# Kernel optimization log

Measured on AMD Instinct MI355X. Metric: run time of the kernel, lower is better.

## Reference

```python
import jax, jax.numpy as jnp
import numpy as np

LAPLACIAN = jnp.array([[-1., -1., -1.], [-1., 8., -1.], [-1., -1., -1.]], dtype=jnp.float32).reshape(1, 1, 3, 3)
AVG5 = jnp.ones((1, 1, 5, 5), dtype=jnp.float32) / 25.0


def _conv_same(x, kernel):
    # x: [B,1,H,W], kernel: [O=1,I=1,kh,kw], SAME padding (odd kernels)
    return jax.lax.conv_general_dilated(
        x, kernel, window_strides=(1, 1), padding='SAME',
        dimension_numbers=('NCHW', 'OIHW', 'NCHW'))


def setup_inputs() -> dict:
    key = jax.random.key(0)
    k0, k1, k2, k3 = jax.random.split(key, 4)
    B, H, W = 16, 1024, 1024
    mask = jax.random.uniform(k0, (B, 1, H, W), dtype=jnp.float32)
    # per-sample params scaled into documented ranges
    blur_strength = 1.0 + 4.0 * jax.random.uniform(k1, (B, 1), dtype=jnp.float32)      # 1.0-5.0
    edge_sensitivity = 0.5 + 1.5 * jax.random.uniform(k2, (B, 1), dtype=jnp.float32)   # 0.5-2.0
    final_threshold = 0.3 + 0.4 * jax.random.uniform(k3, (B, 1), dtype=jnp.float32)    # 0.3-0.7
    return {"mask": mask, "blur_strength": blur_strength,
            "edge_sensitivity": edge_sensitivity, "final_threshold": final_threshold}


def reference(mask, blur_strength, edge_sensitivity, final_threshold):
    B = mask.shape[0]
    edges = jnp.abs(_conv_same(mask, LAPLACIAN))                      # [B,1,H,W]
    edge_threshold = 0.5 * edge_sensitivity.reshape(B, 1, 1, 1)
    edge_mask = (edges > edge_threshold).astype(mask.dtype)
    smoothed_base = _conv_same(mask, AVG5)                            # 5x5 box blur
    blur_factor = blur_strength.reshape(B, 1, 1, 1) / 3.0
    smoothed = mask * (1.0 - blur_factor) + smoothed_base * blur_factor
    result = mask * (1.0 - edge_mask) + smoothed * edge_mask
    final_mask = (result > final_threshold.reshape(B, 1, 1, 1)).astype(mask.dtype)
    return final_mask
```

## Files before the change

kernel.cpp:

```cpp
#include <hip/hip_runtime.h>

#define NB 16
#define HH 1024
#define WW 1024
#define TW 128
#define TH 32
#define LC 136
#define LR 36
#define N4 (LR * (LC / 4))
#define NSTG 5

#define EPS1 2e-4f
#define EPS2 1e-4f

typedef float f32x4 __attribute__((ext_vector_type(4)));

__device__ __noinline__ float aes_exact(const float (*raw)[LC], int lr, int lc,
                                        float bsf, float esf, float fthr)
{
    const double bfd   = (double)bsf / 3.0;
    const double ethrd = 0.5 * (double)esf;
    const double fthrd = (double)fthr;
    const double w25d  = (double)(1.0f / 25.0f);

    double s25 = 0.0, s9 = 0.0;
    for (int dy = 0; dy < 5; ++dy)
        for (int dx = 0; dx < 5; ++dx) {
            double v = (double)raw[lr + dy][lc + dx];
            s25 += v;
            if (dy >= 1 && dy <= 3 && dx >= 1 && dx <= 3) s9 += v;
        }
    double c      = (double)raw[lr + 2][lc + 2];
    double edges  = fabs(9.0 * c - s9);
    double sbase  = s25 * w25d;
    double smooth = c * (1.0 - bfd) + sbase * bfd;
    double result = (edges > ethrd) ? smooth : c;
    return (result > fthrd) ? 1.0f : 0.0f;
}

__global__ __launch_bounds__(256)
void aes_kernel(const float* __restrict__ mask,
                const float* __restrict__ blur_strength,
                const float* __restrict__ edge_sensitivity,
                const float* __restrict__ final_threshold,
                float* __restrict__ out)
{
    __shared__ float raw[2][LR][LC];

    const int b      = blockIdx.z;
    const int tile_y = blockIdx.y * TH;
    const int tx0    = blockIdx.x * (2 * TW);
    const float* m = mask + (size_t)b * (HH * WW);

    const float bsf    = blur_strength[b];
    const float esf    = edge_sensitivity[b];
    const float fthr   = final_threshold[b];
    const float ethr   = 0.5f * esf;
    const float bff    = bsf / 3.0f;
    const float onembf = 1.0f - bff;
    const float w25f   = 1.0f / 25.0f;

    const int tx  = threadIdx.x & 31;
    const int ty  = threadIdx.x >> 5;
    const int lr0 = ty * 4;
    const int lc0 = 4 * tx + 2;

    f32x4 stg[NSTG];

#define STAGE_LOAD(TILE_X)                                                  \
    {                                                                       \
        _Pragma("unroll")                                                   \
        for (int k = 0; k < NSTG; ++k) {                                    \
            int i = (int)threadIdx.x + k * 256;                             \
            f32x4 v = {0.f, 0.f, 0.f, 0.f};                                 \
            if (i < N4) {                                                   \
                int row = i / (LC / 4);                                     \
                int c4  = i - row * (LC / 4);                               \
                int gy  = tile_y - 2 + row;                                 \
                int gx  = (TILE_X) - 4 + 4 * c4;           \
                if ((unsigned)gy < (unsigned)HH && (unsigned)gx < (unsigned)WW) \
                    v = *(const f32x4*)(m + (size_t)gy * WW + gx);          \
            }                                                               \
            stg[k] = v;                                                     \
        }                                                                   \
    }

#define STAGE_WRITE(BUF)                                                    \
    {                                                                       \
        _Pragma("unroll")                                                   \
        for (int k = 0; k < NSTG; ++k) {                                    \
            int i = (int)threadIdx.x + k * 256;                             \
            if (i < N4) {                                                   \
                int row = i / (LC / 4);                                     \
                int c4  = i - row * (LC / 4);                               \
                *(f32x4*)&raw[(BUF)][row][4 * c4] = stg[k];                 \
            }                                                               \
        }                                                                   \
    }

#define LOADROW(RB, ROWIDX, K)                                              \
    {                                                                       \
        const float* rp = &RB[(ROWIDX)][0];                                 \
        float2 u0 = *(const float2*)(rp + lc0);            \
        float4 u1 = *(const float4*)(rp + lc0 + 2);        \
        float2 u2 = *(const float2*)(rp + lc0 + 6);        \
        float a0 = u0.x, a1 = u0.y, a2 = u1.x, a3 = u1.y;                   \
        float a4 = u1.z, a5 = u1.w, a6 = u2.x, a7 = u2.y;                   \
        float s5 = ((a0 + a1) + (a2 + a3)) + a4;                            \
        h5[(K)][0] = s5; s5 = s5 - a0 + a5;                                 \
        h5[(K)][1] = s5; s5 = s5 - a1 + a6;                                 \
        h5[(K)][2] = s5; s5 = s5 - a2 + a7;                                 \
        h5[(K)][3] = s5;                                                    \
        float s3 = (a1 + a2) + a3;                                          \
        h3[(K)][0] = s3; s3 = s3 - a1 + a4;                                 \
        h3[(K)][1] = s3; s3 = s3 - a2 + a5;                                 \
        h3[(K)][2] = s3; s3 = s3 - a3 + a6;                                 \
        h3[(K)][3] = s3;                                                    \
        cc[(K)][0] = a2; cc[(K)][1] = a3; cc[(K)][2] = a4; cc[(K)][3] = a5; \
    }

#define COMPUTE(BUF, TILE_X)                                                \
    {                                                                       \
        const float (*rb)[LC] = raw[(BUF)];                                 \
        float h5[5][4], h3[5][4], cc[5][4];                                 \
        _Pragma("unroll")                                                   \
        for (int k = 0; k < 4; ++k)                                         \
            LOADROW(rb, lr0 + k, k)                                         \
        float* op = out + (size_t)b * (HH * WW)                             \
                        + (size_t)(tile_y + ty * 4) * WW + (TILE_X) + 4 * tx; \
        _Pragma("unroll")                                                   \
        for (int r = 0; r < 4; ++r) {                                       \
            LOADROW(rb, lr0 + r + 4, (r + 4) % 5)                           \
            const int i0 = r % 5, i1 = (r + 1) % 5, i2 = (r + 2) % 5;       \
            const int i3 = (r + 3) % 5, i4 = (r + 4) % 5;                   \
            f32x4 ov;                                                       \
            _Pragma("unroll")                                               \
            for (int c = 0; c < 4; ++c) {                                   \
                float sum25  = ((h5[i0][c] + h5[i1][c])                     \
                              + (h5[i2][c] + h5[i3][c])) + h5[i4][c];       \
                float s9     = h3[i1][c] + h3[i2][c] + h3[i3][c];           \
                float center = cc[i2][c];                                   \
                float edges  = fabsf(9.0f * center - s9);                   \
                float sbase  = sum25 * w25f;                                \
                float smooth = center * onembf + sbase * bff;               \
                bool isedge = edges > ethr;                                 \
                bool conf = (fabsf(edges - ethr) > EPS1) &&                 \
                            (!isedge || (fabsf(smooth - fthr) > EPS2));     \
                float res = isedge ? smooth : center;                       \
                float o   = (res > fthr) ? 1.0f : 0.0f;                     \
                if (!conf)                                                  \
                    o = aes_exact(rb, lr0 + r, lc0 + c, bsf, esf, fthr);    \
                ov[c] = o;                                                  \
            }                                                               \
            __builtin_nontemporal_store(ov, (f32x4*)(op + (size_t)r * WW)); \
        }                                                                   \
    }

    STAGE_LOAD(tx0)
    STAGE_WRITE(0)
    __syncthreads();

    STAGE_LOAD(tx0 + TW)
    COMPUTE(0, tx0)
    STAGE_WRITE(1)
    __syncthreads();

    COMPUTE(1, tx0 + TW)

#undef STAGE_LOAD
#undef STAGE_WRITE
#undef LOADROW
#undef COMPUTE
}

extern "C" void kernel_launch(void* const* d_in, const int* in_sizes, int n_in,
                              void* d_out, int out_size, void* d_ws, size_t ws_size,
                              hipStream_t stream) {
    const float* mask = (const float*)d_in[0];
    const float* bs   = (const float*)d_in[1];
    const float* es   = (const float*)d_in[2];
    const float* ft   = (const float*)d_in[3];
    float* out = (float*)d_out;

    dim3 grid(WW / (2 * TW), HH / TH, NB);
    aes_kernel<<<grid, 256, 0, stream>>>(mask, bs, es, ft, out);
}
```

Before: 36.49 us.

## Process vertical strip of four tiles per block with double-buffered pipeline

Each block now walks a vertical strip of four 32-row tiles, where it previously handled two horizontally adjacent tiles. Global loads for the next tile are issued into registers while the current tile is computed from shared memory. This lengthens the software pipeline and cuts the block count, amortising setup and the first unhidden load. The strip is still not used for halo reuse, since each tile reloads its own 4-row halo. Fewer, longer blocks may hurt load balance and occupancy across CUs.

```diff
diff --git a/kernel.cpp b/kernel.cpp
--- a/kernel.cpp
+++ b/kernel.cpp
@@ -5,6 +5,7 @@
 #define WW 1024
 #define TW 128
 #define TH 32
+#define NT 4
 #define LC 136
 #define LR 36
 #define N4 (LR * (LC / 4))
@@ -47,9 +48,9 @@
 {
     __shared__ float raw[2][LR][LC];
 
-    const int b      = blockIdx.z;
-    const int tile_y = blockIdx.y * TH;
-    const int tx0    = blockIdx.x * (2 * TW);
+    const int b       = blockIdx.z;
+    const int tile_x  = blockIdx.x * TW;
+    const int strip_y = blockIdx.y * (NT * TH);
     const float* m = mask + (size_t)b * (HH * WW);
 
     const float bsf    = blur_strength[b];
@@ -67,8 +68,9 @@
 
     f32x4 stg[NSTG];
 
-#define STAGE_LOAD(TILE_X)                                                  \
+#define STAGE_LOAD(T)                                                       \
     {                                                                       \
+        const int tile_y = strip_y + (T) * TH;                              \
         _Pragma("unroll")                                                   \
         for (int k = 0; k < NSTG; ++k) {                                    \
             int i = (int)threadIdx.x + k * 256;                             \
@@ -77,7 +79,7 @@
                 int row = i / (LC / 4);                                     \
                 int c4  = i - row * (LC / 4);                               \
                 int gy  = tile_y - 2 + row;                                 \
-                int gx  = (TILE_X) - 4 + 4 * c4;           \
+                int gx  = tile_x - 4 + 4 * c4;             \
                 if ((unsigned)gy < (unsigned)HH && (unsigned)gx < (unsigned)WW) \
                     v = *(const f32x4*)(m + (size_t)gy * WW + gx);          \
             }                                                               \
@@ -119,15 +121,16 @@
         cc[(K)][0] = a2; cc[(K)][1] = a3; cc[(K)][2] = a4; cc[(K)][3] = a5; \
     }
 
-#define COMPUTE(BUF, TILE_X)                                                \
+#define COMPUTE(BUF, T)                                                     \
     {                                                                       \
+        const int tile_y = strip_y + (T) * TH;                              \
         const float (*rb)[LC] = raw[(BUF)];                                 \
         float h5[5][4], h3[5][4], cc[5][4];                                 \
         _Pragma("unroll")                                                   \
         for (int k = 0; k < 4; ++k)                                         \
             LOADROW(rb, lr0 + k, k)                                         \
         float* op = out + (size_t)b * (HH * WW)                             \
-                        + (size_t)(tile_y + ty * 4) * WW + (TILE_X) + 4 * tx; \
+                        + (size_t)(tile_y + ty * 4) * WW + tile_x + 4 * tx; \
         _Pragma("unroll")                                                   \
         for (int r = 0; r < 4; ++r) {                                       \
             LOADROW(rb, lr0 + r + 4, (r + 4) % 5)                           \
@@ -156,16 +159,19 @@
         }                                                                   \
     }
 
-    STAGE_LOAD(tx0)
+    STAGE_LOAD(0)
     STAGE_WRITE(0)
     __syncthreads();
 
-    STAGE_LOAD(tx0 + TW)
-    COMPUTE(0, tx0)
-    STAGE_WRITE(1)
-    __syncthreads();
-
-    COMPUTE(1, tx0 + TW)
+    #pragma unroll
+    for (int t = 0; t < NT; ++t) {
+        if (t < NT - 1) STAGE_LOAD(t + 1)
+        COMPUTE(t & 1, t)
+        if (t < NT - 1) {
+            STAGE_WRITE((t + 1) & 1)
+            __syncthreads();
+        }
+    }
 
 #undef STAGE_LOAD
 #undef STAGE_WRITE
@@ -182,6 +188,6 @@
     const float* ft   = (const float*)d_in[3];
     float* out = (float*)d_out;
 
-    dim3 grid(WW / (2 * TW), HH / TH, NB);
+    dim3 grid(WW / TW, HH / (NT * TH), NB);
     aes_kernel<<<grid, 256, 0, stream>>>(mask, bs, es, ft, out);
 }
```

After: 44.69 us. 1.22x slower.

## Use direct global-to-LDS loads for interior blocks and pair tiles vertically

Applied to the files above, without the earlier changes.

Each block now processes two vertically stacked 128x32 tiles instead of two horizontally adjacent ones. Interior blocks fill shared memory with `global_load_lds` direct copies, which skips the staging registers and the bounds checks. Border blocks keep the old register-staged, zero-padded load path. Output stores are deferred until after the barrier and use regular stores instead of nontemporal ones. This adds a divergent code path and depends on the async LDS loads completing before the barrier.

```diff
diff --git a/kernel.cpp b/kernel.cpp
--- a/kernel.cpp
+++ b/kernel.cpp
@@ -7,13 +7,25 @@
 #define TH 32
 #define LC 136
 #define LR 36
-#define N4 (LR * (LC / 4))
-#define NSTG 5
+#define C4 (LC / 4)
+#define N4 (LR * C4)
+#define GRIDX (WW / TW)
+#define GRIDY (HH / (2 * TH))
 
 #define EPS1 2e-4f
 #define EPS2 1e-4f
 
 typedef float f32x4 __attribute__((ext_vector_type(4)));
+
+__device__ __forceinline__ void gload_lds16(const float* g, float* l) {
+#if __has_builtin(__builtin_amdgcn_global_load_lds)
+    __builtin_amdgcn_global_load_lds(
+        (const __attribute__((address_space(1))) void*)g,
+        (__attribute__((address_space(3))) void*)l, 16, 0, 0);
+#else
+    *(f32x4*)l = *(const f32x4*)g;
+#endif
+}
 
 __device__ __noinline__ float aes_exact(const float (*raw)[LC], int lr, int lc,
                                         float bsf, float esf, float fthr)
@@ -48,8 +60,8 @@
     __shared__ float raw[2][LR][LC];
 
     const int b      = blockIdx.z;
-    const int tile_y = blockIdx.y * TH;
-    const int tx0    = blockIdx.x * (2 * TW);
+    const int tile_x = blockIdx.x * TW;
+    const int sy0    = blockIdx.y * (2 * TH);
     const float* m = mask + (size_t)b * (HH * WW);
 
     const float bsf    = blur_strength[b];
@@ -65,19 +77,33 @@
     const int lr0 = ty * 4;
     const int lc0 = 4 * tx + 2;
 
-    f32x4 stg[NSTG];
-
-#define STAGE_LOAD(TILE_X)                                                  \
-    {                                                                       \
-        _Pragma("unroll")                                                   \
-        for (int k = 0; k < NSTG; ++k) {                                    \
+    const bool interior = (blockIdx.x >= 1) & (blockIdx.x <= GRIDX - 2)
+                        & (blockIdx.y >= 1) & (blockIdx.y <= GRIDY - 2);
+
+#define STAGE_DMA(TY, BUF)                                                  \
+    {                                                                       \
+        _Pragma("unroll")                                                   \
+        for (int k = 0; k < 5; ++k) {                                       \
+            int i = (int)threadIdx.x + k * 256;                             \
+            if (i < N4) {                                                   \
+                int row = i / C4, c4 = i - row * C4;                        \
+                gload_lds16(m + (size_t)((TY) - 2 + row) * WW               \
+                              + (tile_x - 4 + 4 * c4),                      \
+                            &raw[(BUF)][0][0] + (size_t)i * 4);             \
+            }                                                               \
+        }                                                                   \
+    }
+
+#define STAGE_LOAD(TY)                                                      \
+    {                                                                       \
+        _Pragma("unroll")                                                   \
+        for (int k = 0; k < 5; ++k) {                                       \
             int i = (int)threadIdx.x + k * 256;                             \
             f32x4 v = {0.f, 0.f, 0.f, 0.f};                                 \
             if (i < N4) {                                                   \
-                int row = i / (LC / 4);                                     \
-                int c4  = i - row * (LC / 4);                               \
-                int gy  = tile_y - 2 + row;                                 \
-                int gx  = (TILE_X) - 4 + 4 * c4;           \
+                int row = i / C4, c4 = i - row * C4;                        \
+                int gy = (TY) - 2 + row;                                    \
+                int gx = tile_x - 4 + 4 * c4;                               \
                 if ((unsigned)gy < (unsigned)HH && (unsigned)gx < (unsigned)WW) \
                     v = *(const f32x4*)(m + (size_t)gy * WW + gx);          \
             }                                                               \
@@ -88,11 +114,10 @@
 #define STAGE_WRITE(BUF)                                                    \
     {                                                                       \
         _Pragma("unroll")                                                   \
-        for (int k = 0; k < NSTG; ++k) {                                    \
+        for (int k = 0; k < 5; ++k) {                                       \
             int i = (int)threadIdx.x + k * 256;                             \
             if (i < N4) {                                                   \
-                int row = i / (LC / 4);                                     \
-                int c4  = i - row * (LC / 4);                               \
+                int row = i / C4, c4 = i - row * C4;                        \
                 *(f32x4*)&raw[(BUF)][row][4 * c4] = stg[k];                 \
             }                                                               \
         }                                                                   \
@@ -119,21 +144,18 @@
         cc[(K)][0] = a2; cc[(K)][1] = a3; cc[(K)][2] = a4; cc[(K)][3] = a5; \
     }
 
-#define COMPUTE(BUF, TILE_X)                                                \
+#define COMPUTE_VALS(BUF, OVV)                                              \
     {                                                                       \
         const float (*rb)[LC] = raw[(BUF)];                                 \
         float h5[5][4], h3[5][4], cc[5][4];                                 \
         _Pragma("unroll")                                                   \
         for (int k = 0; k < 4; ++k)                                         \
             LOADROW(rb, lr0 + k, k)                                         \
-        float* op = out + (size_t)b * (HH * WW)                             \
-                        + (size_t)(tile_y + ty * 4) * WW + (TILE_X) + 4 * tx; \
         _Pragma("unroll")                                                   \
         for (int r = 0; r < 4; ++r) {                                       \
             LOADROW(rb, lr0 + r + 4, (r + 4) % 5)                           \
             const int i0 = r % 5, i1 = (r + 1) % 5, i2 = (r + 2) % 5;       \
             const int i3 = (r + 3) % 5, i4 = (r + 4) % 5;                   \
-            f32x4 ov;                                                       \
             _Pragma("unroll")                                               \
             for (int c = 0; c < 4; ++c) {                                   \
                 float sum25  = ((h5[i0][c] + h5[i1][c])                     \
@@ -150,27 +172,51 @@
                 float o   = (res > fthr) ? 1.0f : 0.0f;                     \
                 if (!conf)                                                  \
                     o = aes_exact(rb, lr0 + r, lc0 + c, bsf, esf, fthr);    \
-                ov[c] = o;                                                  \
-            }                                                               \
-            __builtin_nontemporal_store(ov, (f32x4*)(op + (size_t)r * WW)); \
-        }                                                                   \
-    }
-
-    STAGE_LOAD(tx0)
-    STAGE_WRITE(0)
-    __syncthreads();
-
-    STAGE_LOAD(tx0 + TW)
-    COMPUTE(0, tx0)
-    STAGE_WRITE(1)
-    __syncthreads();
-
-    COMPUTE(1, tx0 + TW)
-
+                OVV[r][c] = o;                                              \
+            }                                                               \
+        }                                                                   \
+    }
+
+#define STORE_VALS(TY, OVV)                                                 \
+    {                                                                       \
+        float* op = out + (size_t)b * (HH * WW)                             \
+                        + (size_t)((TY) + ty * 4) * WW + tile_x + 4 * tx;   \
+        _Pragma("unroll")                                                   \
+        for (int r = 0; r < 4; ++r)                                         \
+            *(f32x4*)(op + (size_t)r * WW) = OVV[r];                        \
+    }
+
+    f32x4 ov0[4], ov1[4];
+
+    if (interior) {
+        STAGE_DMA(sy0, 0)
+        __syncthreads();
+        STAGE_DMA(sy0 + TH, 1)
+        COMPUTE_VALS(0, ov0)
+        __syncthreads();
+        STORE_VALS(sy0, ov0)
+        COMPUTE_VALS(1, ov1)
+        STORE_VALS(sy0 + TH, ov1)
+    } else {
+        f32x4 stg[5];
+        STAGE_LOAD(sy0)
+        STAGE_WRITE(0)
+        __syncthreads();
+        STAGE_LOAD(sy0 + TH)
+        COMPUTE_VALS(0, ov0)
+        STAGE_WRITE(1)
+        __syncthreads();
+        STORE_VALS(sy0, ov0)
+        COMPUTE_VALS(1, ov1)
+        STORE_VALS(sy0 + TH, ov1)
+    }
+
+#undef STAGE_DMA
 #undef STAGE_LOAD
 #undef STAGE_WRITE
 #undef LOADROW
-#undef COMPUTE
+#undef COMPUTE_VALS
+#undef STORE_VALS
 }
 
 extern "C" void kernel_launch(void* const* d_in, const int* in_sizes, int n_in,
@@ -182,6 +228,6 @@
     const float* ft   = (const float*)d_in[3];
     float* out = (float*)d_out;
 
-    dim3 grid(WW / (2 * TW), HH / TH, NB);
+    dim3 grid(GRIDX, GRIDY, NB);
     aes_kernel<<<grid, 256, 0, stream>>>(mask, bs, es, ft, out);
 }
```

Result: slower. 41.39 us (+13.4%).
